# Optimization experiments

Measured on AMD Instinct MI355X. Metric: run time of the kernel, lower is better.

## Reference

```python
import jax, jax.numpy as jnp
import numpy as np

EMB_DIM = 256
HEAD_DIM = 32


def setup_inputs() -> dict:
    key = jax.random.key(0)
    kx, kq, kk, kv = jax.random.split(key, 4)
    B, S = 4, 4096
    x = jax.random.normal(kx, (B, S, EMB_DIM), dtype=jnp.float32)
    # Linear(emb_dim, head_dim, bias=False): store as [emb_dim, head_dim]
    sc = 1.0 / np.sqrt(EMB_DIM)
    Wq = jax.random.normal(kq, (EMB_DIM, HEAD_DIM), dtype=jnp.float32) * sc
    Wk = jax.random.normal(kk, (EMB_DIM, HEAD_DIM), dtype=jnp.float32) * sc
    Wv = jax.random.normal(kv, (EMB_DIM, HEAD_DIM), dtype=jnp.float32) * sc
    return {"x": x, "Wq": Wq, "Wk": Wk, "Wv": Wv}


def reference(x, Wq, Wk, Wv):
    # single-head attention with POST-softmax scaling (as in source).
    # Dropout treated as identity (eval mode) for determinism.
    scaling = HEAD_DIM ** (-0.5)
    q = jnp.einsum('bse,ed->bsd', x, Wq)
    k = jnp.einsum('bse,ed->bsd', x, Wk)
    v = jnp.einsum('bse,ed->bsd', x, Wv)
    energy = jnp.einsum('bqd,bkd->bqk', q, k)  # [B,S,S]
    att = jax.nn.softmax(energy, axis=-1) * scaling
    out = jnp.einsum('bqk,bkd->bqd', att, v)
    return out
```

## Files before the change

### kernel.cpp

```cpp
#include <hip/hip_runtime.h>

#define EMB 256
#define HD 32
#define SEQ 4096
#define NSPLIT 8
#define KRANGE 512
#define NQROW 16384

typedef _Float16 half8 __attribute__((ext_vector_type(8)));
typedef float floatx4 __attribute__((ext_vector_type(4)));

#define L2E 1.44269504088896340736f
#define SCALING 0.17677669529663687f

__device__ __forceinline__ void xpose2(unsigned x, unsigned y, unsigned& o0, unsigned& o1) {
  int lane = threadIdx.x & 63;
  int n = lane & 15, quad = lane >> 4;
  int a0 = (n + 32 * (quad & 1)) << 2;
  int a1 = (n + 16 + 32 * (quad & 1)) << 2;
  unsigned t0 = (unsigned)__builtin_amdgcn_ds_bpermute(a0, (int)x);
  unsigned t1 = (unsigned)__builtin_amdgcn_ds_bpermute(a0, (int)y);
  o0 = (quad < 2) ? t0 : t1;
  unsigned t2 = (unsigned)__builtin_amdgcn_ds_bpermute(a1, (int)x);
  unsigned t3 = (unsigned)__builtin_amdgcn_ds_bpermute(a1, (int)y);
  o1 = (quad < 2) ? t2 : t3;
}

__device__ __forceinline__ float crossmax(float x) {
  x = fmaxf(x, __shfl_xor(x, 16));
  return fmaxf(x, __shfl_xor(x, 32));
}

__device__ __forceinline__ half8 mk8(unsigned a, unsigned b, unsigned c, unsigned d) {
  union { unsigned u[4]; half8 h; } z;
  z.u[0] = a; z.u[1] = b; z.u[2] = c; z.u[3] = d;
  return z.h;
}

__global__ __launch_bounds__(256) void prep_kernel(const float* __restrict__ Wq,
                                                   const float* __restrict__ Wk,
                                                   const float* __restrict__ Wv,
                                                   _Float16* __restrict__ wsw) {
  int gid = blockIdx.x * 256 + threadIdx.x;
  int j    = gid & 7;
  int lane = (gid >> 3) & 63;
  int kc   = (gid >> 9) & 7;
  int half = (gid >> 12) & 1;
  int mat  = gid >> 13;
  const float* W = (mat == 0) ? Wq : ((mat == 1) ? Wk : Wv);
  int n = lane & 15, quad = lane >> 4;
  int e = kc * 32 + quad * 8 + j;
  int d = n + half * 16;
  float v = W[e * HD + d];
  if (mat == 0) v *= L2E;
  wsw[gid] = (_Float16)v;
}

__global__ __launch_bounds__(256) void qkv_kernel(const float* __restrict__ x,
                                                  const _Float16* __restrict__ wsw,
                                                  _Float16* __restrict__ qw,
                                                  _Float16* __restrict__ kw,
                                                  _Float16* __restrict__ vt) {
  int lane = threadIdx.x & 63, wave = threadIdx.x >> 6;
  int n = lane & 15, quad = lane >> 4;
  int rowbase = blockIdx.x * 64 + wave * 16;

  floatx4 c[3][2];
#pragma unroll
  for (int m = 0; m < 3; ++m)
#pragma unroll
    for (int h = 0; h < 2; ++h) c[m][h] = (floatx4){0, 0, 0, 0};

#pragma unroll
  for (int kc = 0; kc < 8; ++kc) {
    const float* xp = x + (rowbase + n) * EMB + kc * 32 + quad * 8;
    float4 xa = *(const float4*)(xp);
    float4 xb = *(const float4*)(xp + 4);
    half8 a;
    a[0] = (_Float16)xa.x; a[1] = (_Float16)xa.y; a[2] = (_Float16)xa.z; a[3] = (_Float16)xa.w;
    a[4] = (_Float16)xb.x; a[5] = (_Float16)xb.y; a[6] = (_Float16)xb.z; a[7] = (_Float16)xb.w;
#pragma unroll
    for (int m = 0; m < 3; ++m)
#pragma unroll
      for (int h = 0; h < 2; ++h) {
        half8 bb = *(const half8*)(wsw + (((m * 2 + h) * 8 + kc) << 9) + (lane << 3));
        c[m][h] = __builtin_amdgcn_mfma_f32_16x16x32_f16(a, bb, c[m][h], 0, 0, 0);
      }
  }

#pragma unroll
  for (int r = 0; r < 4; ++r) {
    int row = rowbase + quad * 4 + r;
    qw[row * HD + n]      = (_Float16)c[0][0][r];
    qw[row * HD + n + 16] = (_Float16)c[0][1][r];
    kw[row * HD + n]      = (_Float16)c[1][0][r];
    kw[row * HD + n + 16] = (_Float16)c[1][1][r];
  }
  int b = rowbase >> 12;
  int s0 = rowbase & (SEQ - 1);
  _Float16* vb = vt + b * HD * SEQ;
#pragma unroll
  for (int r = 0; r < 4; ++r) {
    int s = s0 + quad * 4 + r;
    vb[n * SEQ + s]        = (_Float16)c[2][0][r];
    vb[(n + 16) * SEQ + s] = (_Float16)c[2][1][r];
  }
}

__global__ __launch_bounds__(256) void attn_kernel(const _Float16* __restrict__ q,
                                                   const _Float16* __restrict__ k,
                                                   const _Float16* __restrict__ vt,
                                                   float* __restrict__ Op,
                                                   float* __restrict__ Mp,
                                                   float* __restrict__ Lp) {
  const int t = threadIdx.x;
  const int w = t >> 6, lane = t & 63;
  const int n = lane & 15, quad = lane >> 4;
  const int qb = blockIdx.x & 127;
  const int sp = blockIdx.x >> 7;
  const int b = qb >> 5;
  const int qrow0 = qb * 128 + w * 32;
  const int key0 = sp * KRANGE;

  const _Float16* kb = k  + (size_t)(b * SEQ + key0) * HD;
  const _Float16* vb = vt + (size_t)b * HD * SEQ + key0;

  half8 qf0 = *(const half8*)(q + (qrow0 + n) * HD + quad * 8);
  half8 qf1 = *(const half8*)(q + (qrow0 + 16 + n) * HD + quad * 8);

  half8 aone = {0,0,0,0,0,0,0,0};
  if (n == 0) { aone[0]=1; aone[1]=1; aone[2]=1; aone[3]=1; aone[4]=1; aone[5]=1; aone[6]=1; aone[7]=1; }

  floatx4 o00 = {0,0,0,0}, o01 = {0,0,0,0};
  floatx4 o10 = {0,0,0,0}, o11 = {0,0,0,0};
  floatx4 l0 = {0,0,0,0}, l1 = {0,0,0,0};
  float m0 = -__builtin_huge_valf(), m1 = -__builtin_huge_valf();
  const floatx4 zero = {0,0,0,0};

#pragma unroll 2
  for (int kt = 0; kt < KRANGE / 64; ++kt) {
    const _Float16* kt0 = kb + kt * 64 * HD;
    const _Float16* vt0 = vb + kt * 64;
    half8 ka0 = *(const half8*)(kt0 + (n)      * HD + quad * 8);
    half8 ka1 = *(const half8*)(kt0 + (16 + n) * HD + quad * 8);
    half8 ka2 = *(const half8*)(kt0 + (32 + n) * HD + quad * 8);
    half8 ka3 = *(const half8*)(kt0 + (48 + n) * HD + quad * 8);
    half8 va00 = *(const half8*)(vt0 + (n)      * SEQ + quad * 8);
    half8 va01 = *(const half8*)(vt0 + (16 + n) * SEQ + quad * 8);
    half8 va10 = *(const half8*)(vt0 + (n)      * SEQ + 32 + quad * 8);
    half8 va11 = *(const half8*)(vt0 + (16 + n) * SEQ + 32 + quad * 8);

    floatx4 s0[4], s1[4];
    s0[0] = __builtin_amdgcn_mfma_f32_16x16x32_f16(ka0, qf0, zero, 0, 0, 0);
    s0[1] = __builtin_amdgcn_mfma_f32_16x16x32_f16(ka1, qf0, zero, 0, 0, 0);
    s0[2] = __builtin_amdgcn_mfma_f32_16x16x32_f16(ka2, qf0, zero, 0, 0, 0);
    s0[3] = __builtin_amdgcn_mfma_f32_16x16x32_f16(ka3, qf0, zero, 0, 0, 0);
    s1[0] = __builtin_amdgcn_mfma_f32_16x16x32_f16(ka0, qf1, zero, 0, 0, 0);
    s1[1] = __builtin_amdgcn_mfma_f32_16x16x32_f16(ka1, qf1, zero, 0, 0, 0);
    s1[2] = __builtin_amdgcn_mfma_f32_16x16x32_f16(ka2, qf1, zero, 0, 0, 0);
    s1[3] = __builtin_amdgcn_mfma_f32_16x16x32_f16(ka3, qf1, zero, 0, 0, 0);

    half8 B00, B01, B10, B11;
#pragma unroll
    for (int c = 0; c < 2; ++c) {
      floatx4* sv = c ? s1 : s0;
      float& mr = c ? m1 : m0;
      floatx4 t01 = __builtin_elementwise_max(sv[0], sv[1]);
      floatx4 t23 = __builtin_elementwise_max(sv[2], sv[3]);
      floatx4 t4  = __builtin_elementwise_max(t01, t23);
      float mm = fmaxf(fmaxf(t4[0], t4[1]), fmaxf(t4[2], t4[3]));
      mm = crossmax(mm);
      float mnew = fmaxf(mr, mm);
      float alpha = __builtin_amdgcn_exp2f(mr - mnew);
      mr = mnew;

      unsigned pk[4][2];
#pragma unroll
      for (int g = 0; g < 4; ++g) {
        float p0 = __builtin_amdgcn_exp2f(sv[g][0] - mnew);
        float p1 = __builtin_amdgcn_exp2f(sv[g][1] - mnew);
        float p2 = __builtin_amdgcn_exp2f(sv[g][2] - mnew);
        float p3 = __builtin_amdgcn_exp2f(sv[g][3] - mnew);
        pk[g][0] = __builtin_bit_cast(unsigned, __builtin_amdgcn_cvt_pkrtz(p0, p1));
        pk[g][1] = __builtin_bit_cast(unsigned, __builtin_amdgcn_cvt_pkrtz(p2, p3));
      }
      unsigned b00, b02, b01, b03, b10, b12, b11, b13;
      xpose2(pk[0][0], pk[1][0], b00, b02);
      xpose2(pk[0][1], pk[1][1], b01, b03);
      xpose2(pk[2][0], pk[3][0], b10, b12);
      xpose2(pk[2][1], pk[3][1], b11, b13);
      if (c == 0) {
        B00 = mk8(b00, b01, b02, b03); B01 = mk8(b10, b11, b12, b13);
        o00 *= alpha; o01 *= alpha; l0[0] *= alpha;
      } else {
        B10 = mk8(b00, b01, b02, b03); B11 = mk8(b10, b11, b12, b13);
        o10 *= alpha; o11 *= alpha; l1[0] *= alpha;
      }
    }

    o00 = __builtin_amdgcn_mfma_f32_16x16x32_f16(va00, B00, o00, 0, 0, 0);
    o00 = __builtin_amdgcn_mfma_f32_16x16x32_f16(va10, B01, o00, 0, 0, 0);
    o01 = __builtin_amdgcn_mfma_f32_16x16x32_f16(va01, B00, o01, 0, 0, 0);
    o01 = __builtin_amdgcn_mfma_f32_16x16x32_f16(va11, B01, o01, 0, 0, 0);
    l0  = __builtin_amdgcn_mfma_f32_16x16x32_f16(aone, B00, l0, 0, 0, 0);
    l0  = __builtin_amdgcn_mfma_f32_16x16x32_f16(aone, B01, l0, 0, 0, 0);

    o10 = __builtin_amdgcn_mfma_f32_16x16x32_f16(va00, B10, o10, 0, 0, 0);
    o10 = __builtin_amdgcn_mfma_f32_16x16x32_f16(va10, B11, o10, 0, 0, 0);
    o11 = __builtin_amdgcn_mfma_f32_16x16x32_f16(va01, B10, o11, 0, 0, 0);
    o11 = __builtin_amdgcn_mfma_f32_16x16x32_f16(va11, B11, o11, 0, 0, 0);
    l1  = __builtin_amdgcn_mfma_f32_16x16x32_f16(aone, B10, l1, 0, 0, 0);
    l1  = __builtin_amdgcn_mfma_f32_16x16x32_f16(aone, B11, l1, 0, 0, 0);
  }

  size_t obase = ((size_t)(sp * NQROW + qrow0)) * 32;
  *(floatx4*)&Op[obase + (size_t)n * 32 + quad * 4]             = o00;
  *(floatx4*)&Op[obase + (size_t)n * 32 + 16 + quad * 4]        = o01;
  *(floatx4*)&Op[obase + (size_t)(16 + n) * 32 + quad * 4]      = o10;
  *(floatx4*)&Op[obase + (size_t)(16 + n) * 32 + 16 + quad * 4] = o11;
  if (quad == 0) {
    int mi = sp * NQROW + qrow0;
    Mp[mi + n]      = m0;
    Mp[mi + 16 + n] = m1;
    Lp[mi + n]      = l0[0];
    Lp[mi + 16 + n] = l1[0];
  }
}

__global__ __launch_bounds__(256) void combine_kernel(const float* __restrict__ Op,
                                                      const float* __restrict__ Mp,
                                                      const float* __restrict__ Lp,
                                                      float* __restrict__ out) {
  int gid = blockIdx.x * 256 + threadIdx.x;
  int d = gid & 31, qrow = gid >> 5;
  float mv[NSPLIT];
  float ms = -__builtin_huge_valf();
#pragma unroll
  for (int sp = 0; sp < NSPLIT; ++sp) {
    mv[sp] = Mp[sp * NQROW + qrow];
    ms = fmaxf(ms, mv[sp]);
  }
  float L = 0.f, O = 0.f;
#pragma unroll
  for (int sp = 0; sp < NSPLIT; ++sp) {
    float ww = __builtin_amdgcn_exp2f(mv[sp] - ms);
    L += ww * Lp[sp * NQROW + qrow];
    O += ww * Op[((size_t)(sp * NQROW + qrow)) * 32 + d];
  }
  out[gid] = O * SCALING / L;
}

extern "C" void kernel_launch(void* const* d_in, const int* in_sizes, int n_in,
                              void* d_out, int out_size, void* d_ws, size_t ws_size,
                              hipStream_t stream) {
  const float* x  = (const float*)d_in[0];
  const float* Wq = (const float*)d_in[1];
  const float* Wk = (const float*)d_in[2];
  const float* Wv = (const float*)d_in[3];
  float* out = (float*)d_out;

  _Float16* wsw = (_Float16*)d_ws;
  _Float16* qw  = wsw + 24576;
  _Float16* kw  = qw + NQROW * HD;
  _Float16* vt  = kw + NQROW * HD;
  float* Op = (float*)(vt + NQROW * HD);
  float* Mp = Op + (size_t)NSPLIT * NQROW * 32;
  float* Lp = Mp + NSPLIT * NQROW;

  prep_kernel<<<96, 256, 0, stream>>>(Wq, Wk, Wv, wsw);
  qkv_kernel<<<256, 256, 0, stream>>>(x, wsw, qw, kw, vt);
  attn_kernel<<<1024, 256, 0, stream>>>(qw, kw, vt, Op, Mp, Lp);
  combine_kernel<<<2048, 256, 0, stream>>>(Op, Mp, Lp, out);
}
```

Measured before the change: 114.0 us.

## Split QKV projection across grid, store partials in fp16, vectorize combine

The QKV projection grid gains a second dimension so each block computes only one of Q, K or V, giving three times as many blocks at the cost of re-reading x three times. The attention kernel stores its split partial outputs in fp16 instead of fp32, halving that intermediate traffic, and gets a launch-bounds occupancy hint plus a fully unrolled key loop. The combine kernel reads four fp16 values per thread and writes float4 outputs, using a quarter as many threads. Storing partial outputs in fp16 adds some rounding error to the result.

```diff
diff --git a/kernel.cpp b/kernel.cpp
--- a/kernel.cpp
+++ b/kernel.cpp
@@ -8,6 +8,7 @@
 #define NQROW 16384
 
 typedef _Float16 half8 __attribute__((ext_vector_type(8)));
+typedef _Float16 half4v __attribute__((ext_vector_type(4)));
 typedef float floatx4 __attribute__((ext_vector_type(4)));
 
 #define L2E 1.44269504088896340736f
@@ -63,13 +64,10 @@
                                                   _Float16* __restrict__ vt) {
   int lane = threadIdx.x & 63, wave = threadIdx.x >> 6;
   int n = lane & 15, quad = lane >> 4;
+  int mat = blockIdx.y;
   int rowbase = blockIdx.x * 64 + wave * 16;
 
-  floatx4 c[3][2];
-#pragma unroll
-  for (int m = 0; m < 3; ++m)
-#pragma unroll
-    for (int h = 0; h < 2; ++h) c[m][h] = (floatx4){0, 0, 0, 0};
+  floatx4 c0 = {0,0,0,0}, c1 = {0,0,0,0};
 
 #pragma unroll
   for (int kc = 0; kc < 8; ++kc) {
@@ -79,40 +77,39 @@
     half8 a;
     a[0] = (_Float16)xa.x; a[1] = (_Float16)xa.y; a[2] = (_Float16)xa.z; a[3] = (_Float16)xa.w;
     a[4] = (_Float16)xb.x; a[5] = (_Float16)xb.y; a[6] = (_Float16)xb.z; a[7] = (_Float16)xb.w;
-#pragma unroll
-    for (int m = 0; m < 3; ++m)
-#pragma unroll
-      for (int h = 0; h < 2; ++h) {
-        half8 bb = *(const half8*)(wsw + (((m * 2 + h) * 8 + kc) << 9) + (lane << 3));
-        c[m][h] = __builtin_amdgcn_mfma_f32_16x16x32_f16(a, bb, c[m][h], 0, 0, 0);
-      }
-  }
-
-#pragma unroll
-  for (int r = 0; r < 4; ++r) {
-    int row = rowbase + quad * 4 + r;
-    qw[row * HD + n]      = (_Float16)c[0][0][r];
-    qw[row * HD + n + 16] = (_Float16)c[0][1][r];
-    kw[row * HD + n]      = (_Float16)c[1][0][r];
-    kw[row * HD + n + 16] = (_Float16)c[1][1][r];
-  }
-  int b = rowbase >> 12;
-  int s0 = rowbase & (SEQ - 1);
-  _Float16* vb = vt + b * HD * SEQ;
-#pragma unroll
-  for (int r = 0; r < 4; ++r) {
-    int s = s0 + quad * 4 + r;
-    vb[n * SEQ + s]        = (_Float16)c[2][0][r];
-    vb[(n + 16) * SEQ + s] = (_Float16)c[2][1][r];
-  }
-}
-
-__global__ __launch_bounds__(256) void attn_kernel(const _Float16* __restrict__ q,
-                                                   const _Float16* __restrict__ k,
-                                                   const _Float16* __restrict__ vt,
-                                                   float* __restrict__ Op,
-                                                   float* __restrict__ Mp,
-                                                   float* __restrict__ Lp) {
+    half8 b0 = *(const half8*)(wsw + (((mat * 2 + 0) * 8 + kc) << 9) + (lane << 3));
+    half8 b1 = *(const half8*)(wsw + (((mat * 2 + 1) * 8 + kc) << 9) + (lane << 3));
+    c0 = __builtin_amdgcn_mfma_f32_16x16x32_f16(a, b0, c0, 0, 0, 0);
+    c1 = __builtin_amdgcn_mfma_f32_16x16x32_f16(a, b1, c1, 0, 0, 0);
+  }
+
+  if (mat == 2) {
+    int b = rowbase >> 12;
+    int s0 = rowbase & (SEQ - 1);
+    _Float16* vb = vt + b * HD * SEQ;
+#pragma unroll
+    for (int r = 0; r < 4; ++r) {
+      int s = s0 + quad * 4 + r;
+      vb[n * SEQ + s]        = (_Float16)c0[r];
+      vb[(n + 16) * SEQ + s] = (_Float16)c1[r];
+    }
+  } else {
+    _Float16* dst = (mat == 0) ? qw : kw;
+#pragma unroll
+    for (int r = 0; r < 4; ++r) {
+      int row = rowbase + quad * 4 + r;
+      dst[row * HD + n]      = (_Float16)c0[r];
+      dst[row * HD + n + 16] = (_Float16)c1[r];
+    }
+  }
+}
+
+__global__ __launch_bounds__(256, 4) void attn_kernel(const _Float16* __restrict__ q,
+                                                      const _Float16* __restrict__ k,
+                                                      const _Float16* __restrict__ vt,
+                                                      _Float16* __restrict__ Op,
+                                                      float* __restrict__ Mp,
+                                                      float* __restrict__ Lp) {
   const int t = threadIdx.x;
   const int w = t >> 6, lane = t & 63;
   const int n = lane & 15, quad = lane >> 4;
@@ -137,7 +134,7 @@
   float m0 = -__builtin_huge_valf(), m1 = -__builtin_huge_valf();
   const floatx4 zero = {0,0,0,0};
 
-#pragma unroll 2
+#pragma unroll
   for (int kt = 0; kt < KRANGE / 64; ++kt) {
     const _Float16* kt0 = kb + kt * 64 * HD;
     const _Float16* vt0 = vb + kt * 64;
@@ -213,11 +210,17 @@
     l1  = __builtin_amdgcn_mfma_f32_16x16x32_f16(aone, B11, l1, 0, 0, 0);
   }
 
+  half4v p00, p01, p10, p11;
+#pragma unroll
+  for (int r = 0; r < 4; ++r) {
+    p00[r] = (_Float16)o00[r]; p01[r] = (_Float16)o01[r];
+    p10[r] = (_Float16)o10[r]; p11[r] = (_Float16)o11[r];
+  }
   size_t obase = ((size_t)(sp * NQROW + qrow0)) * 32;
-  *(floatx4*)&Op[obase + (size_t)n * 32 + quad * 4]             = o00;
-  *(floatx4*)&Op[obase + (size_t)n * 32 + 16 + quad * 4]        = o01;
-  *(floatx4*)&Op[obase + (size_t)(16 + n) * 32 + quad * 4]      = o10;
-  *(floatx4*)&Op[obase + (size_t)(16 + n) * 32 + 16 + quad * 4] = o11;
+  *(half4v*)&Op[obase + (size_t)n * 32 + quad * 4]             = p00;
+  *(half4v*)&Op[obase + (size_t)n * 32 + 16 + quad * 4]        = p01;
+  *(half4v*)&Op[obase + (size_t)(16 + n) * 32 + quad * 4]      = p10;
+  *(half4v*)&Op[obase + (size_t)(16 + n) * 32 + 16 + quad * 4] = p11;
   if (quad == 0) {
     int mi = sp * NQROW + qrow0;
     Mp[mi + n]      = m0;
@@ -227,12 +230,12 @@
   }
 }
 
-__global__ __launch_bounds__(256) void combine_kernel(const float* __restrict__ Op,
+__global__ __launch_bounds__(256) void combine_kernel(const _Float16* __restrict__ Op,
                                                       const float* __restrict__ Mp,
                                                       const float* __restrict__ Lp,
                                                       float* __restrict__ out) {
   int gid = blockIdx.x * 256 + threadIdx.x;
-  int d = gid & 31, qrow = gid >> 5;
+  int dc = gid & 7, qrow = gid >> 3;
   float mv[NSPLIT];
   float ms = -__builtin_huge_valf();
 #pragma unroll
@@ -240,14 +243,19 @@
     mv[sp] = Mp[sp * NQROW + qrow];
     ms = fmaxf(ms, mv[sp]);
   }
-  float L = 0.f, O = 0.f;
+  float L = 0.f;
+  floatx4 O = {0.f, 0.f, 0.f, 0.f};
 #pragma unroll
   for (int sp = 0; sp < NSPLIT; ++sp) {
     float ww = __builtin_amdgcn_exp2f(mv[sp] - ms);
     L += ww * Lp[sp * NQROW + qrow];
-    O += ww * Op[((size_t)(sp * NQROW + qrow)) * 32 + d];
-  }
-  out[gid] = O * SCALING / L;
+    half4v ov = *(const half4v*)&Op[((size_t)(sp * NQROW + qrow)) * 32 + dc * 4];
+#pragma unroll
+    for (int r = 0; r < 4; ++r) O[r] += ww * (float)ov[r];
+  }
+  float inv = SCALING / L;
+  floatx4 res = {O[0] * inv, O[1] * inv, O[2] * inv, O[3] * inv};
+  *(floatx4*)&out[qrow * HD + dc * 4] = res;
 }
 
 extern "C" void kernel_launch(void* const* d_in, const int* in_sizes, int n_in,
@@ -263,12 +271,12 @@
   _Float16* qw  = wsw + 24576;
   _Float16* kw  = qw + NQROW * HD;
   _Float16* vt  = kw + NQROW * HD;
-  float* Op = (float*)(vt + NQROW * HD);
-  float* Mp = Op + (size_t)NSPLIT * NQROW * 32;
+  _Float16* Op  = vt + NQROW * HD;
+  float* Mp = (float*)(Op + (size_t)NSPLIT * NQROW * 32);
   float* Lp = Mp + NSPLIT * NQROW;
 
   prep_kernel<<<96, 256, 0, stream>>>(Wq, Wk, Wv, wsw);
-  qkv_kernel<<<256, 256, 0, stream>>>(x, wsw, qw, kw, vt);
+  qkv_kernel<<<dim3(256, 3), 256, 0, stream>>>(x, wsw, qw, kw, vt);
   attn_kernel<<<1024, 256, 0, stream>>>(qw, kw, vt, Op, Mp, Lp);
-  combine_kernel<<<2048, 256, 0, stream>>>(Op, Mp, Lp, out);
-}
+  combine_kernel<<<512, 256, 0, stream>>>(Op, Mp, Lp, out);
+}
```

Result: faster. 106.0 us (-7.0%).
